# Kernel tuning notes

Hardware: AMD Instinct MI355X
Metric: run time of the kernel (lower is better)

## Reference

```python
import jax, jax.numpy as jnp
import numpy as np

H = 2048        # hidden_size
E = 64          # num_experts
TOPK = 4        # top_k_experts
EPS = 1e-6      # rms_norm_eps
SW = 1024       # sliding_window
NEG = jnp.finfo(jnp.float32).min


def setup_inputs() -> dict:
    key = jax.random.key(0)
    k1, k2, k3, k4, k5 = jax.random.split(key, 5)
    B, S = 2, 4096
    x = jax.random.normal(k1, (B, S, H), jnp.float32)
    # 1-based document ids packed contiguously; 0 = padding
    packed_seq_ids = jnp.sort(jax.random.randint(k2, (B, S), 0, 5), axis=-1)
    # 0 = text, 1/2 = vision tokens
    mm_token_type_ids = jax.random.randint(k3, (B, S), 0, 3)
    scale = jax.random.uniform(k4, (H,), jnp.float32, 0.5, 1.5)
    proj_w = jax.random.normal(k5, (E, H), jnp.float32) * 0.02
    return dict(x=x, packed_seq_ids=packed_seq_ids,
                mm_token_type_ids=mm_token_type_ids, scale=scale, proj_w=proj_w)


def _vision_group_ids(mm):
    # per-image-block ids for vision tokens, -1 for text/padding
    is_v = (mm == 1) | (mm == 2)
    is_prev = jnp.concatenate([jnp.zeros_like(is_v[:, :1]), is_v[:, :-1]], axis=-1)
    starts = is_v & ~is_prev
    gid = jnp.cumsum(starts.astype(jnp.int32), axis=1) - 1
    return jnp.where(is_v, gid, -1)


def _build_masks(packed, mm, sliding_window):
    B, S = packed.shape
    pos = jnp.arange(S)
    causal = pos[None, :, None] >= pos[None, None, :]          # [1,S,S] kv<=q
    valid_q = packed[:, :, None] > 0
    valid_kv = packed[:, None, :] > 0
    same_doc = (packed[:, :, None] == packed[:, None, :]) & valid_q & valid_kv
    full = same_doc & causal                                   # [B,S,S]
    sliding = full & ((pos[None, :, None] - pos[None, None, :]) < sliding_window)
    gid = _vision_group_ids(mm)
    same_vg = (gid[:, :, None] == gid[:, None, :]) & (gid[:, :, None] >= 0)
    sliding = (sliding | same_vg) & same_doc
    # additive format, [B,1,S,S]
    full_add = jnp.where(full[:, None], jnp.float32(0.0), NEG)
    sliding_add = jnp.where(sliding[:, None], jnp.float32(0.0), NEG)
    return full_add, sliding_add


def _gate(x, scale, proj_w):
    # Gemma4Gate: RMSNorm(no scale) -> H**-0.5 -> learnable scale -> linear
    #             -> softmax -> top-k -> renormalize
    xf = x.reshape(-1, H)                                      # [N,H]
    xn = xf * jax.lax.rsqrt(jnp.mean(xf * xf, axis=-1, keepdims=True) + EPS)
    xn = xn * (H ** -0.5) * scale
    logits = jnp.einsum('nh,eh->ne', xn, proj_w)               # [N,E]
    probs = jax.nn.softmax(logits, axis=-1)
    weights, indices = jax.lax.top_k(probs, TOPK)              # [N,K]
    weights = weights / jnp.maximum(jnp.sum(weights, axis=-1, keepdims=True), 1e-20)
    return weights, indices


def reference(x, packed_seq_ids, mm_token_type_ids, scale, proj_w):
    full_mask, sliding_mask = _build_masks(packed_seq_ids, mm_token_type_ids, SW)
    weights, indices = _gate(x, scale, proj_w)
    return full_mask, sliding_mask, weights, indices
```

## Files before the change

### kernel.cpp

```cpp
#include <hip/hip_runtime.h>
#include <math.h>

#define S 4096
#define HH 2048
#define NE 64
#define SW 1024
#define MASKED 0xFBFFu

typedef unsigned short u16;
typedef unsigned int u32;
typedef _Float16 f16;
typedef f16 f16x8 __attribute__((ext_vector_type(8)));
typedef float f32x4 __attribute__((ext_vector_type(4)));

__device__ __align__(16) int g_gid[2 * S];
__device__ __align__(16) u16 g_pwB[NE * HH];

__device__ __forceinline__ float h2f(u32 lo16) {
    union { u16 u; f16 h; } v; v.u = (u16)lo16; return (float)v.h;
}
__device__ __forceinline__ u16 f2h(float f) {
    union { u16 u; f16 h; } v; v.h = (f16)f; return v.u;
}

__global__ __launch_bounds__(256) void pre_kernel(const int* __restrict__ mm,
                                                  const u16* __restrict__ proj_w,
                                                  const u16* __restrict__ scale) {
    const int blk = blockIdx.x;
    const int t = threadIdx.x;
    if (blk < 2) {
        __shared__ int ts[256];
        const int* m = mm + blk * S;
        const int base_pos = t * 16;
        int vals[16];
#pragma unroll
        for (int i = 0; i < 16; i++) vals[i] = m[base_pos + i];
        bool prevv = false;
        if (base_pos > 0) {
            int pv = m[base_pos - 1];
            prevv = (pv == 1) || (pv == 2);
        }
        int cnt = 0;
        {
            bool pv = prevv;
#pragma unroll
            for (int i = 0; i < 16; i++) {
                bool is = (vals[i] == 1) || (vals[i] == 2);
                cnt += (is && !pv) ? 1 : 0;
                pv = is;
            }
        }
        ts[t] = cnt;
        __syncthreads();
        for (int off = 1; off < 256; off <<= 1) {
            int add = (t >= off) ? ts[t - off] : 0;
            __syncthreads();
            ts[t] += add;
            __syncthreads();
        }
        int base = ts[t] - cnt;
        {
            bool pv = prevv;
            int run = base;
#pragma unroll
            for (int i = 0; i < 16; i++) {
                bool is = (vals[i] == 1) || (vals[i] == 2);
                run += (is && !pv) ? 1 : 0;
                g_gid[blk * S + base_pos + i] = is ? (run - 1) : -1;
                pv = is;
            }
        }
    } else {
        int idx = (blk - 2) * 256 + t;
        int e = idx >> 11;
        int h = idx & 2047;
        float v = h2f((u32)proj_w[idx]) * h2f((u32)scale[h]);
        int ch2 = h >> 5;
        int lrow = (h >> 3) & 3;
        int j = h & 7;
        int eg = e >> 4;
        int ecol = e & 15;
        g_pwB[(size_t)(((ch2 * 4 + eg) * 64) + lrow * 16 + ecol) * 8 + j] = f2h(v);
    }
}

__global__ __launch_bounds__(256) void fused_kernel(
    const u16* __restrict__ x, const int* __restrict__ packed,
    u16* __restrict__ full_out, u16* __restrict__ slid_out,
    u16* __restrict__ w_out, u16* __restrict__ i_out) {

    __shared__ float lg[64][65];

    const int t = threadIdx.x;

    if (blockIdx.x >= 128) {
        const int tid = (blockIdx.x - 128) * 256 + t;
        const int kc = tid & 511;
        const int q = (tid >> 9) & 4095;
        const int b = tid >> 21;
        const int k0 = kc * 8;

        const int pq = packed[b * S + q];
        const int gq = g_gid[b * S + q];
        const int4 pk0 = *(const int4*)(packed + b * S + k0);
        const int4 pk1 = *(const int4*)(packed + b * S + k0 + 4);
        const int4 gk0 = *(const int4*)(g_gid + b * S + k0);
        const int4 gk1 = *(const int4*)(g_gid + b * S + k0 + 4);

        int pkj[8] = {pk0.x, pk0.y, pk0.z, pk0.w, pk1.x, pk1.y, pk1.z, pk1.w};
        int gkj[8] = {gk0.x, gk0.y, gk0.z, gk0.w, gk1.x, gk1.y, gk1.z, gk1.w};
        u32 fm[8], sm[8];
#pragma unroll
        for (int j = 0; j < 8; j++) {
            int k = k0 + j;
            bool sd = (pq > 0) && (pkj[j] == pq);
            bool fl = sd && (q >= k);
            bool sl = ((fl && ((q - k) < SW)) || ((gkj[j] == gq) && (gq >= 0))) && sd;
            fm[j] = fl ? 0u : MASKED;
            sm[j] = sl ? 0u : MASKED;
        }
        uint4 f4, s4;
        f4.x = fm[0] | (fm[1] << 16); f4.y = fm[2] | (fm[3] << 16);
        f4.z = fm[4] | (fm[5] << 16); f4.w = fm[6] | (fm[7] << 16);
        s4.x = sm[0] | (sm[1] << 16); s4.y = sm[2] | (sm[3] << 16);
        s4.z = sm[4] | (sm[5] << 16); s4.w = sm[6] | (sm[7] << 16);

        size_t off = (size_t)b * ((size_t)S * S) + (size_t)q * S + k0;
        *(uint4*)(full_out + off) = f4;
        *(uint4*)(slid_out + off) = s4;
        return;
    }

    const int w = t >> 6;
    const int l = t & 63;
    const int tok0 = blockIdx.x * 64;
    const int m16 = l & 15;
    const int kq = l >> 4;

    const uint4* ap = (const uint4*)(x + (size_t)(tok0 + w * 16 + m16) * HH);
    const uint4* bp = (const uint4*)g_pwB;

    f32x4 acc0 = {0.f, 0.f, 0.f, 0.f};
    f32x4 acc1 = {0.f, 0.f, 0.f, 0.f};
    f32x4 acc2 = {0.f, 0.f, 0.f, 0.f};
    f32x4 acc3 = {0.f, 0.f, 0.f, 0.f};
    float ss = 0.0f;

#pragma unroll 4
    for (int ch2 = 0; ch2 < 64; ++ch2) {
        union { uint4 u; f16x8 h; } a, b0, b1, b2, b3;
        a.u = ap[ch2 * 4 + kq];
        b0.u = bp[(ch2 * 4 + 0) * 64 + l];
        b1.u = bp[(ch2 * 4 + 1) * 64 + l];
        b2.u = bp[(ch2 * 4 + 2) * 64 + l];
        b3.u = bp[(ch2 * 4 + 3) * 64 + l];
#pragma unroll
        for (int j = 0; j < 8; j++) {
            float xf = (float)a.h[j];
            ss += xf * xf;
        }
        acc0 = __builtin_amdgcn_mfma_f32_16x16x32_f16(a.h, b0.h, acc0, 0, 0, 0);
        acc1 = __builtin_amdgcn_mfma_f32_16x16x32_f16(a.h, b1.h, acc1, 0, 0, 0);
        acc2 = __builtin_amdgcn_mfma_f32_16x16x32_f16(a.h, b2.h, acc2, 0, 0, 0);
        acc3 = __builtin_amdgcn_mfma_f32_16x16x32_f16(a.h, b3.h, acc3, 0, 0, 0);
    }

    ss += __shfl_xor(ss, 16);
    ss += __shfl_xor(ss, 32);
    float fac = rsqrtf(ss * (1.0f / 2048.0f) + 1e-6f) * 0.022097086912079608f;

#pragma unroll
    for (int r = 0; r < 4; r++) {
        int m = 4 * kq + r;
        float fm = __shfl(fac, m);
        lg[w * 16 + m][0 + m16]  = acc0[r] * fm;
        lg[w * 16 + m][16 + m16] = acc1[r] * fm;
        lg[w * 16 + m][32 + m16] = acc2[r] * fm;
        lg[w * 16 + m][48 + m16] = acc3[r] * fm;
    }
    __syncthreads();

    if (t < 64) {
        unsigned long long used = 0ull;
        float bv[4];
        int bi[4];
#pragma unroll
        for (int p = 0; p < 4; p++) {
            float best = -INFINITY;
            int besti = 0;
            for (int e = 0; e < NE; e++) {
                if (used & (1ull << e)) continue;
                float v = lg[t][e];
                if (v > best) { best = v; besti = e; }
            }
            used |= 1ull << besti;
            bv[p] = best;
            bi[p] = besti;
        }
        float ww[4];
        float ssum = 0.0f;
#pragma unroll
        for (int p = 0; p < 4; p++) { ww[p] = expf(bv[p] - bv[0]); ssum += ww[p]; }
        int n = tok0 + t;
#pragma unroll
        for (int p = 0; p < 4; p++) {
            w_out[n * 4 + p] = f2h(ww[p] / ssum);
            i_out[n * 4 + p] = f2h((float)bi[p]);
        }
    }
}

extern "C" void kernel_launch(void* const* d_in, const int* in_sizes, int n_in,
                              void* d_out, int out_size, void* d_ws, size_t ws_size,
                              hipStream_t stream) {
    const u16* x = (const u16*)d_in[0];
    const int* packed = (const int*)d_in[1];
    const int* mm = (const int*)d_in[2];
    const u16* scale = (const u16*)d_in[3];
    const u16* proj_w = (const u16*)d_in[4];

    u16* out = (u16*)d_out;
    u16* full_out = out;
    u16* slid_out = out + 33554432;
    u16* w_out = out + 67108864;
    u16* i_out = out + 67141632;

    pre_kernel<<<514, 256, 0, stream>>>(mm, proj_w, scale);
    fused_kernel<<<128 + 16384, 256, 0, stream>>>(x, packed,
                                                  full_out, slid_out, w_out, i_out);
    (void)in_sizes; (void)n_in; (void)out_size; (void)d_ws; (void)ws_size;
}
```

Measured before the change: 308.7 us.

## Use one block per mask row with nontemporal stores and drop the weight pre-pack

```diff
diff --git a/kernel.cpp b/kernel.cpp
--- a/kernel.cpp
+++ b/kernel.cpp
@@ -12,9 +12,9 @@
 typedef _Float16 f16;
 typedef f16 f16x8 __attribute__((ext_vector_type(8)));
 typedef float f32x4 __attribute__((ext_vector_type(4)));
+typedef u32 u32x4 __attribute__((ext_vector_type(4)));
 
 __device__ __align__(16) int g_gid[2 * S];
-__device__ __align__(16) u16 g_pwB[NE * HH];
 
 __device__ __forceinline__ float h2f(u32 lo16) {
     union { u16 u; f16 h; } v; v.u = (u16)lo16; return (float)v.h;
@@ -23,69 +23,55 @@
     union { u16 u; f16 h; } v; v.h = (f16)f; return v.u;
 }
 
-__global__ __launch_bounds__(256) void pre_kernel(const int* __restrict__ mm,
-                                                  const u16* __restrict__ proj_w,
-                                                  const u16* __restrict__ scale) {
+__global__ __launch_bounds__(256) void pre_kernel(const int* __restrict__ mm) {
     const int blk = blockIdx.x;
     const int t = threadIdx.x;
-    if (blk < 2) {
-        __shared__ int ts[256];
-        const int* m = mm + blk * S;
-        const int base_pos = t * 16;
-        int vals[16];
-#pragma unroll
-        for (int i = 0; i < 16; i++) vals[i] = m[base_pos + i];
-        bool prevv = false;
-        if (base_pos > 0) {
-            int pv = m[base_pos - 1];
-            prevv = (pv == 1) || (pv == 2);
-        }
-        int cnt = 0;
-        {
-            bool pv = prevv;
-#pragma unroll
-            for (int i = 0; i < 16; i++) {
-                bool is = (vals[i] == 1) || (vals[i] == 2);
-                cnt += (is && !pv) ? 1 : 0;
-                pv = is;
-            }
-        }
-        ts[t] = cnt;
+    __shared__ int ts[256];
+    const int* m = mm + blk * S;
+    const int base_pos = t * 16;
+    int vals[16];
+#pragma unroll
+    for (int i = 0; i < 16; i++) vals[i] = m[base_pos + i];
+    bool prevv = false;
+    if (base_pos > 0) {
+        int pv = m[base_pos - 1];
+        prevv = (pv == 1) || (pv == 2);
+    }
+    int cnt = 0;
+    {
+        bool pv = prevv;
+#pragma unroll
+        for (int i = 0; i < 16; i++) {
+            bool is = (vals[i] == 1) || (vals[i] == 2);
+            cnt += (is && !pv) ? 1 : 0;
+            pv = is;
+        }
+    }
+    ts[t] = cnt;
+    __syncthreads();
+    for (int off = 1; off < 256; off <<= 1) {
+        int add = (t >= off) ? ts[t - off] : 0;
         __syncthreads();
-        for (int off = 1; off < 256; off <<= 1) {
-            int add = (t >= off) ? ts[t - off] : 0;
-            __syncthreads();
-            ts[t] += add;
-            __syncthreads();
-        }
-        int base = ts[t] - cnt;
-        {
-            bool pv = prevv;
-            int run = base;
-#pragma unroll
-            for (int i = 0; i < 16; i++) {
-                bool is = (vals[i] == 1) || (vals[i] == 2);
-                run += (is && !pv) ? 1 : 0;
-                g_gid[blk * S + base_pos + i] = is ? (run - 1) : -1;
-                pv = is;
-            }
-        }
-    } else {
-        int idx = (blk - 2) * 256 + t;
-        int e = idx >> 11;
-        int h = idx & 2047;
-        float v = h2f((u32)proj_w[idx]) * h2f((u32)scale[h]);
-        int ch2 = h >> 5;
-        int lrow = (h >> 3) & 3;
-        int j = h & 7;
-        int eg = e >> 4;
-        int ecol = e & 15;
-        g_pwB[(size_t)(((ch2 * 4 + eg) * 64) + lrow * 16 + ecol) * 8 + j] = f2h(v);
+        ts[t] += add;
+        __syncthreads();
+    }
+    int base = ts[t] - cnt;
+    {
+        bool pv = prevv;
+        int run = base;
+#pragma unroll
+        for (int i = 0; i < 16; i++) {
+            bool is = (vals[i] == 1) || (vals[i] == 2);
+            run += (is && !pv) ? 1 : 0;
+            g_gid[blk * S + base_pos + i] = is ? (run - 1) : -1;
+            pv = is;
+        }
     }
 }
 
 __global__ __launch_bounds__(256) void fused_kernel(
-    const u16* __restrict__ x, const int* __restrict__ packed,
+    const u16* __restrict__ x, const u16* __restrict__ scale,
+    const u16* __restrict__ proj_w, const int* __restrict__ packed,
     u16* __restrict__ full_out, u16* __restrict__ slid_out,
     u16* __restrict__ w_out, u16* __restrict__ i_out) {
 
@@ -94,40 +80,43 @@
     const int t = threadIdx.x;
 
     if (blockIdx.x >= 128) {
-        const int tid = (blockIdx.x - 128) * 256 + t;
-        const int kc = tid & 511;
-        const int q = (tid >> 9) & 4095;
-        const int b = tid >> 21;
-        const int k0 = kc * 8;
+        const int blk = blockIdx.x - 128;
+        const int q = blk & 4095;
+        const int b = blk >> 12;
 
         const int pq = packed[b * S + q];
         const int gq = g_gid[b * S + q];
-        const int4 pk0 = *(const int4*)(packed + b * S + k0);
-        const int4 pk1 = *(const int4*)(packed + b * S + k0 + 4);
-        const int4 gk0 = *(const int4*)(g_gid + b * S + k0);
-        const int4 gk1 = *(const int4*)(g_gid + b * S + k0 + 4);
-
-        int pkj[8] = {pk0.x, pk0.y, pk0.z, pk0.w, pk1.x, pk1.y, pk1.z, pk1.w};
-        int gkj[8] = {gk0.x, gk0.y, gk0.z, gk0.w, gk1.x, gk1.y, gk1.z, gk1.w};
-        u32 fm[8], sm[8];
-#pragma unroll
-        for (int j = 0; j < 8; j++) {
-            int k = k0 + j;
-            bool sd = (pq > 0) && (pkj[j] == pq);
-            bool fl = sd && (q >= k);
-            bool sl = ((fl && ((q - k) < SW)) || ((gkj[j] == gq) && (gq >= 0))) && sd;
-            fm[j] = fl ? 0u : MASKED;
-            sm[j] = sl ? 0u : MASKED;
-        }
-        uint4 f4, s4;
-        f4.x = fm[0] | (fm[1] << 16); f4.y = fm[2] | (fm[3] << 16);
-        f4.z = fm[4] | (fm[5] << 16); f4.w = fm[6] | (fm[7] << 16);
-        s4.x = sm[0] | (sm[1] << 16); s4.y = sm[2] | (sm[3] << 16);
-        s4.z = sm[4] | (sm[5] << 16); s4.w = sm[6] | (sm[7] << 16);
-
-        size_t off = (size_t)b * ((size_t)S * S) + (size_t)q * S + k0;
-        *(uint4*)(full_out + off) = f4;
-        *(uint4*)(slid_out + off) = s4;
+
+#pragma unroll
+        for (int half = 0; half < 2; half++) {
+            const int k0 = t * 8 + half * 2048;
+            const int4 pk0 = *(const int4*)(packed + b * S + k0);
+            const int4 pk1 = *(const int4*)(packed + b * S + k0 + 4);
+            const int4 gk0 = *(const int4*)(g_gid + b * S + k0);
+            const int4 gk1 = *(const int4*)(g_gid + b * S + k0 + 4);
+
+            int pkj[8] = {pk0.x, pk0.y, pk0.z, pk0.w, pk1.x, pk1.y, pk1.z, pk1.w};
+            int gkj[8] = {gk0.x, gk0.y, gk0.z, gk0.w, gk1.x, gk1.y, gk1.z, gk1.w};
+            u32 fm[8], sm[8];
+#pragma unroll
+            for (int j = 0; j < 8; j++) {
+                int k = k0 + j;
+                bool sd = (pq > 0) && (pkj[j] == pq);
+                bool fl = sd && (q >= k);
+                bool sl = ((fl && ((q - k) < SW)) || ((gkj[j] == gq) && (gq >= 0))) && sd;
+                fm[j] = fl ? 0u : MASKED;
+                sm[j] = sl ? 0u : MASKED;
+            }
+            u32x4 f4, s4;
+            f4.x = fm[0] | (fm[1] << 16); f4.y = fm[2] | (fm[3] << 16);
+            f4.z = fm[4] | (fm[5] << 16); f4.w = fm[6] | (fm[7] << 16);
+            s4.x = sm[0] | (sm[1] << 16); s4.y = sm[2] | (sm[3] << 16);
+            s4.z = sm[4] | (sm[5] << 16); s4.w = sm[6] | (sm[7] << 16);
+
+            size_t off = (size_t)b * ((size_t)S * S) + (size_t)q * S + k0;
+            __builtin_nontemporal_store(f4, (u32x4*)(full_out + off));
+            __builtin_nontemporal_store(s4, (u32x4*)(slid_out + off));
+        }
         return;
     }
 
@@ -138,7 +127,8 @@
     const int kq = l >> 4;
 
     const uint4* ap = (const uint4*)(x + (size_t)(tok0 + w * 16 + m16) * HH);
-    const uint4* bp = (const uint4*)g_pwB;
+    const uint4* sp = (const uint4*)scale;
+    const uint4* bp = (const uint4*)proj_w;
 
     f32x4 acc0 = {0.f, 0.f, 0.f, 0.f};
     f32x4 acc1 = {0.f, 0.f, 0.f, 0.f};
@@ -148,17 +138,20 @@
 
 #pragma unroll 4
     for (int ch2 = 0; ch2 < 64; ++ch2) {
-        union { uint4 u; f16x8 h; } a, b0, b1, b2, b3;
-        a.u = ap[ch2 * 4 + kq];
-        b0.u = bp[(ch2 * 4 + 0) * 64 + l];
-        b1.u = bp[(ch2 * 4 + 1) * 64 + l];
-        b2.u = bp[(ch2 * 4 + 2) * 64 + l];
-        b3.u = bp[(ch2 * 4 + 3) * 64 + l];
+        union { uint4 u; f16x8 h; } a, sv, b0, b1, b2, b3;
+        const int hq = ch2 * 4 + kq;
+        a.u = ap[hq];
+        sv.u = sp[hq];
+        b0.u = bp[(size_t)(0 * 16 + m16) * 256 + hq];
+        b1.u = bp[(size_t)(1 * 16 + m16) * 256 + hq];
+        b2.u = bp[(size_t)(2 * 16 + m16) * 256 + hq];
+        b3.u = bp[(size_t)(3 * 16 + m16) * 256 + hq];
 #pragma unroll
         for (int j = 0; j < 8; j++) {
             float xf = (float)a.h[j];
             ss += xf * xf;
         }
+        a.h = a.h * sv.h;
         acc0 = __builtin_amdgcn_mfma_f32_16x16x32_f16(a.h, b0.h, acc0, 0, 0, 0);
         acc1 = __builtin_amdgcn_mfma_f32_16x16x32_f16(a.h, b1.h, acc1, 0, 0, 0);
         acc2 = __builtin_amdgcn_mfma_f32_16x16x32_f16(a.h, b2.h, acc2, 0, 0, 0);
@@ -225,8 +218,8 @@
     u16* w_out = out + 67108864;
     u16* i_out = out + 67141632;
 
-    pre_kernel<<<514, 256, 0, stream>>>(mm, proj_w, scale);
-    fused_kernel<<<128 + 16384, 256, 0, stream>>>(x, packed,
-                                                  full_out, slid_out, w_out, i_out);
+    pre_kernel<<<2, 256, 0, stream>>>(mm);
+    fused_kernel<<<128 + 8192, 256, 0, stream>>>(x, scale, proj_w, packed,
+                                                 full_out, slid_out, w_out, i_out);
     (void)in_sizes; (void)n_in; (void)out_size; (void)d_ws; (void)ws_size;
 }
```

After: 319.1 us. 3.4% more time.
